# Performance work log

Measured on AMD Instinct MI355X. Metric: run time of the kernel, lower is better.

Reference implementation:

```python
import jax, jax.numpy as jnp
import numpy as np

N_NODES = 50000
N_EDGES = 800000
IN_DIM, HIDDEN, OUT_DIM = 256, 128, 64
N_LAYERS = 2
NEG_SLOPE = 0.1


def setup_inputs() -> dict:
    key = jax.random.key(0)
    ks = jax.random.split(key, 10)
    x = jax.random.normal(ks[0], (N_NODES, IN_DIM), dtype=jnp.float32)
    edge_index = jax.random.randint(ks[1], (2, N_EDGES), 0, N_NODES, dtype=jnp.int64)
    s = 1.0 / np.sqrt(IN_DIM)
    enc_W = jax.random.uniform(ks[2], (IN_DIM, HIDDEN), jnp.float32, -s, s)
    enc_b = jax.random.uniform(ks[3], (HIDDEN,), jnp.float32, -s, s)
    sh = 1.0 / np.sqrt(HIDDEN)
    conv_W = jax.random.uniform(ks[4], (N_LAYERS, HIDDEN, HIDDEN), jnp.float32, -sh, sh)
    conv_b = jnp.zeros((N_LAYERS, HIDDEN), dtype=jnp.float32)
    dec_W = jax.random.uniform(ks[5], (HIDDEN, OUT_DIM), jnp.float32, -sh, sh)
    dec_b = jax.random.uniform(ks[6], (OUT_DIM,), jnp.float32, -sh, sh)
    return {"x": x, "edge_index": edge_index, "enc_W": enc_W, "enc_b": enc_b,
            "conv_W": conv_W, "conv_b": conv_b, "dec_W": dec_W, "dec_b": dec_b}


def _gcn_norm(edge_index, num_nodes):
    # PyG gcn_norm with add_self_loops=True, edge_weight=1
    loops = jnp.arange(num_nodes, dtype=edge_index.dtype)
    src = jnp.concatenate([edge_index[0], loops])
    dst = jnp.concatenate([edge_index[1], loops])
    deg = jax.ops.segment_sum(jnp.ones_like(dst, dtype=jnp.float32), dst,
                              num_segments=num_nodes)
    dinv = jnp.where(deg > 0, jax.lax.rsqrt(deg), 0.0)
    norm = dinv[src] * dinv[dst]  # [E+N]
    return src, dst, norm


def _gcn_conv(h, W, b, src, dst, norm, num_nodes):
    h = h @ W                       # [N, H] dense transform (no bias in lin)
    msg = h[src] * norm[:, None]    # gather + scale, [E+N, H]
    out = jax.ops.segment_sum(msg, dst, num_segments=num_nodes)  # scatter-add
    return out + b


def reference(x, edge_index, enc_W, enc_b, conv_W, conv_b, dec_W, dec_b):
    n = x.shape[0]
    src, dst, norm = _gcn_norm(edge_index, n)
    # eval mode: F.dropout(training=False) is identity
    h = jax.nn.leaky_relu(x @ enc_W + enc_b, NEG_SLOPE)
    for i in range(N_LAYERS):
        h = jax.nn.leaky_relu(_gcn_conv(h, conv_W[i], conv_b[i], src, dst, norm, n),
                              NEG_SLOPE)
    return h @ dec_W + dec_b
```

## Files before the change

kernel.cpp:

```cpp
#include <hip/hip_runtime.h>


constexpr int HID = 128;
constexpr float NEG = 0.1f;
constexpr int CAP = 96;
constexpr int FILL_BLKS = 256;
constexpr int CSTR = 8;

typedef __attribute__((ext_vector_type(8))) short short8;
typedef __attribute__((ext_vector_type(4))) float f32x4;

union frag8 { short8 s; unsigned u[4]; };

__device__ __forceinline__ float lrelu(float v) { return v > 0.f ? v : v * NEG; }

__device__ __forceinline__ unsigned fbits(float f) {
  union { float f; unsigned u; } c; c.f = f; return c.u;
}
__device__ __forceinline__ unsigned short f2bf(float f) {
  unsigned u = fbits(f);
  return (unsigned short)((u + 0x7fffu + ((u >> 16) & 1u)) >> 16);
}
__device__ __forceinline__ float bf2f(unsigned short h) {
  union { unsigned u; float f; } c; c.u = ((unsigned)h) << 16; return c.f;
}

__device__ __forceinline__ void gload16(const unsigned short* g, unsigned short* l) {
  __builtin_amdgcn_global_load_lds((const __attribute__((address_space(1))) unsigned*)g,
                                   (__attribute__((address_space(3))) unsigned*)l, 16, 0, 0);
}

__global__ __launch_bounds__(256) void k_pre(const float* __restrict__ encW,
                                             const float* __restrict__ convW,
                                             const float* __restrict__ decW,
                                             unsigned short* __restrict__ wf_enc,
                                             unsigned short* __restrict__ wf_c0,
                                             unsigned short* __restrict__ wf_c1,
                                             unsigned short* __restrict__ wf_dec,
                                             int* __restrict__ cursor, int N) {
  if (blockIdx.x < 36) {
    int idx = blockIdx.x * 256 + threadIdx.x;
    const float* W; unsigned short* wf; int WN, NT, base, PL;
    if (idx < 4096)      { W = encW;          wf = wf_enc; WN = 128; NT = 8; base = idx;        PL = 32768; }
    else if (idx < 6144) { W = convW;         wf = wf_c0;  WN = 128; NT = 8; base = idx - 4096; PL = 16384; }
    else if (idx < 8192) { W = convW + 16384; wf = wf_c1;  WN = 128; NT = 8; base = idx - 6144; PL = 16384; }
    else if (idx < 9216) { W = decW;          wf = wf_dec; WN = 64;  NT = 4; base = idx - 8192; PL = 8192; }
    else return;
    int lane = base & 63, tile = base >> 6;
    int nt = tile % NT, ks = tile / NT;
    int col = nt * 16 + (lane & 15);
    int krow = ks * 32 + (lane >> 4) * 8;
    unsigned short* ohi = wf + (size_t)base * 8;
    unsigned short* olo = ohi + PL;
#pragma unroll
    for (int j = 0; j < 8; ++j) {
      float v = W[(size_t)(krow + j) * WN + col];
      unsigned short hi = f2bf(v);
      ohi[j] = hi;
      olo[j] = f2bf(v - bf2f(hi));
    }
    return;
  }
  int i = (blockIdx.x - 36) * 256 + threadIdx.x;
  if (i < N) cursor[i * CSTR] = 0;
}

__global__ __launch_bounds__(512) void k_enc_fill(
    const float* __restrict__ A, const unsigned short* __restrict__ wf,
    const float* __restrict__ bias, const int* __restrict__ src,
    const int* __restrict__ dst, int E, int* __restrict__ cursor,
    unsigned short* __restrict__ eidx2, float* __restrict__ h, int M, int encB) {
  __shared__ unsigned short lwf[32768];
  if (blockIdx.x >= encB) {
    int g = blockIdx.x & 7;
    int rk = (blockIdx.x - encB) >> 3;
    int lo = (int)(((long long)g * M) >> 3);
    int hi = (int)(((long long)(g + 1) * M) >> 3);
    for (int e = rk * 512 + threadIdx.x; e < E; e += 32 * 512) {
      int d = dst[e];
      if (d >= lo && d < hi) {
        int pos = atomicAdd(&cursor[d * CSTR], 1);
        if (pos < CAP) eidx2[(size_t)d * CAP + pos] = (unsigned short)src[e];
      }
    }
    return;
  }
  constexpr int NT = 8;
  const int wave = threadIdx.x >> 6, lane = threadIdx.x & 63;
  const int q = lane >> 4, c16 = lane & 15;
  const int row0 = blockIdx.x * 128 + wave * 16;
  int r = row0 + c16;
  if (r >= M) r = M - 1;
  const float* ap = A + (size_t)r * 256 + q * 8;
  f32x4 acc[NT];
#pragma unroll
  for (int nt = 0; nt < NT; ++nt) acc[nt] = (f32x4){0.f, 0.f, 0.f, 0.f};
  float av[8];
  *(float4*)&av[0] = *(const float4*)(ap);
  *(float4*)&av[4] = *(const float4*)(ap + 4);
  for (int half = 0; half < 2; ++half) {
    if (half) __syncthreads();
#pragma unroll
    for (int i = 0; i < 8; ++i) {
      int c = wave + i * 8;
      const unsigned short* s = (c < 32)
          ? wf + half * 16384 + c * 512
          : wf + 32768 + half * 16384 + (c - 32) * 512;
      gload16(s + lane * 8, lwf + c * 512);
    }
    asm volatile("s_waitcnt vmcnt(0)" ::: "memory");
    __syncthreads();
    for (int ksl = 0; ksl < 4; ++ksl) {
      frag8 ahi, alo;
      float res[8];
#pragma unroll
      for (int i = 0; i < 8; ++i) {
        union { unsigned u; float f; } t; t.u = fbits(av[i]) & 0xffff0000u;
        res[i] = av[i] - t.f;
      }
#pragma unroll
      for (int j = 0; j < 4; ++j) {
        ahi.u[j] = __builtin_amdgcn_perm(fbits(av[2 * j + 1]), fbits(av[2 * j]),
                                         0x07060302u);
        alo.u[j] = __builtin_amdgcn_perm(fbits(res[2 * j + 1]), fbits(res[2 * j]),
                                         0x07060302u);
      }
      int ks = half * 4 + ksl;
      if (ks + 1 < 8) {
        *(float4*)&av[0] = *(const float4*)(ap + (ks + 1) * 32);
        *(float4*)&av[4] = *(const float4*)(ap + (ks + 1) * 32 + 4);
      }
      const unsigned short* wph = lwf + ksl * NT * 512 + lane * 8;
#pragma unroll
      for (int nt = 0; nt < NT; ++nt) {
        short8 bhi = *(const short8*)(wph);
        short8 blo = *(const short8*)(wph + 16384);
        acc[nt] = __builtin_amdgcn_mfma_f32_16x16x32_bf16(ahi.s, bhi, acc[nt], 0, 0, 0);
        acc[nt] = __builtin_amdgcn_mfma_f32_16x16x32_bf16(ahi.s, blo, acc[nt], 0, 0, 0);
        acc[nt] = __builtin_amdgcn_mfma_f32_16x16x32_bf16(alo.s, bhi, acc[nt], 0, 0, 0);
        wph += 512;
      }
    }
  }
  float bv[NT];
#pragma unroll
  for (int nt = 0; nt < NT; ++nt) bv[nt] = bias[nt * 16 + c16];
#pragma unroll
  for (int rr = 0; rr < 4; ++rr) {
    int gr = row0 + q * 4 + rr;
    if (gr >= M) continue;
#pragma unroll
    for (int nt = 0; nt < NT; ++nt)
      h[(size_t)gr * 128 + nt * 16 + c16] = lrelu(acc[nt][rr] + bv[nt]);
  }
}

template <int NT, int KS, int MODE>
__global__ __launch_bounds__(512) void k_mfma(const float* __restrict__ A,
                                              const unsigned short* __restrict__ wf,
                                              const float* __restrict__ bias,
                                              const int* __restrict__ deg,
                                              void* __restrict__ Cout, int M) {
  constexpr int K = KS * 32;
  constexpr int NOUT = NT * 16;
  constexpr int PL = KS * NT * 512;
  constexpr int CH = KS * NT * 2;
  __shared__ unsigned short lwf[2 * PL];
  const int wave = threadIdx.x >> 6, lane = threadIdx.x & 63;
  const int q = lane >> 4, c16 = lane & 15;
  const int row0 = blockIdx.x * 128 + wave * 16;
  int r = row0 + c16;
  if (r >= M) r = M - 1;
  const float* ap = A + (size_t)r * K + q * 8;
  f32x4 acc[NT];
#pragma unroll
  for (int nt = 0; nt < NT; ++nt) acc[nt] = (f32x4){0.f, 0.f, 0.f, 0.f};
  float av[8];
  *(float4*)&av[0] = *(const float4*)(ap);
  *(float4*)&av[4] = *(const float4*)(ap + 4);
#pragma unroll
  for (int i = 0; i < CH / 8; ++i) {
    int c = wave + i * 8;
    gload16(wf + c * 512 + lane * 8, lwf + c * 512);
  }
  asm volatile("s_waitcnt vmcnt(0)" ::: "memory");
  __syncthreads();
  for (int ks = 0; ks < KS; ++ks) {
    frag8 ahi, alo;
    float res[8];
#pragma unroll
    for (int i = 0; i < 8; ++i) {
      union { unsigned u; float f; } t; t.u = fbits(av[i]) & 0xffff0000u;
      res[i] = av[i] - t.f;
    }
#pragma unroll
    for (int j = 0; j < 4; ++j) {
      ahi.u[j] = __builtin_amdgcn_perm(fbits(av[2 * j + 1]), fbits(av[2 * j]),
                                       0x07060302u);
      alo.u[j] = __builtin_amdgcn_perm(fbits(res[2 * j + 1]), fbits(res[2 * j]),
                                       0x07060302u);
    }
    if (ks + 1 < KS) {
      *(float4*)&av[0] = *(const float4*)(ap + (ks + 1) * 32);
      *(float4*)&av[4] = *(const float4*)(ap + (ks + 1) * 32 + 4);
    }
    const unsigned short* wph = lwf + ks * NT * 512 + lane * 8;
#pragma unroll
    for (int nt = 0; nt < NT; ++nt) {
      short8 bhi = *(const short8*)(wph);
      short8 blo = *(const short8*)(wph + PL);
      acc[nt] = __builtin_amdgcn_mfma_f32_16x16x32_bf16(ahi.s, bhi, acc[nt], 0, 0, 0);
      acc[nt] = __builtin_amdgcn_mfma_f32_16x16x32_bf16(ahi.s, blo, acc[nt], 0, 0, 0);
      acc[nt] = __builtin_amdgcn_mfma_f32_16x16x32_bf16(alo.s, bhi, acc[nt], 0, 0, 0);
      wph += 512;
    }
  }
  float bv[NT];
  if (MODE == 2) {
#pragma unroll
    for (int nt = 0; nt < NT; ++nt) bv[nt] = bias[nt * 16 + c16];
  }
#pragma unroll
  for (int rr = 0; rr < 4; ++rr) {
    int gr = row0 + q * 4 + rr;
    if (gr >= M) continue;
    if (MODE == 1) {
      float dv = rsqrtf((float)deg[gr * CSTR] + 1.0f);
#pragma unroll
      for (int nt = 0; nt < NT; ++nt)
        ((unsigned short*)Cout)[(size_t)gr * NOUT + nt * 16 + c16] =
            f2bf(acc[nt][rr] * dv);
    } else {
#pragma unroll
      for (int nt = 0; nt < NT; ++nt)
        ((float*)Cout)[(size_t)gr * NOUT + nt * 16 + c16] = acc[nt][rr] + bv[nt];
    }
  }
}

__global__ __launch_bounds__(256) void k_gather(const int* __restrict__ deg,
                                                const unsigned short* __restrict__ eidx2,
                                                const unsigned short* __restrict__ t,
                                                const float* __restrict__ bias,
                                                float* __restrict__ h, int N) {
  int node = (blockIdx.x * 256 + threadIdx.x) >> 4;
  int lane = threadIdx.x & 15;
  if (node >= N) return;
  const uint4* t4 = (const uint4*)t;
  int dtrue = deg[node * CSTR];
  int d = dtrue > CAP ? CAP : dtrue;
  const unsigned short* ep = eidx2 + (size_t)node * CAP;
  float acc[8] = {};
#define ADDV(v)                                         \
  {                                                     \
    unsigned dw[4] = {(v).x, (v).y, (v).z, (v).w};      \
    _Pragma("unroll") for (int i = 0; i < 4; ++i) {     \
      union { unsigned u; float f; } lo, hi;            \
      lo.u = dw[i] << 16;                               \
      hi.u = dw[i] & 0xffff0000u;                       \
      acc[2 * i] += lo.f;                               \
      acc[2 * i + 1] += hi.f;                           \
    }                                                   \
  }
  {
    uint4 vs = t4[(size_t)node * 16 + lane];
    ADDV(vs);
  }
  int e = 0;
  for (; e + 8 <= d; e += 8) {
    int4 sa = *(const int4*)(ep + e);
    unsigned s0 = (unsigned)sa.x & 0xffffu, s1 = (unsigned)sa.x >> 16;
    unsigned s2 = (unsigned)sa.y & 0xffffu, s3 = (unsigned)sa.y >> 16;
    unsigned s4 = (unsigned)sa.z & 0xffffu, s5 = (unsigned)sa.z >> 16;
    unsigned s6 = (unsigned)sa.w & 0xffffu, s7 = (unsigned)sa.w >> 16;
    uint4 v0 = t4[(size_t)s0 * 16 + lane];
    uint4 v1 = t4[(size_t)s1 * 16 + lane];
    uint4 v2 = t4[(size_t)s2 * 16 + lane];
    uint4 v3 = t4[(size_t)s3 * 16 + lane];
    uint4 v4 = t4[(size_t)s4 * 16 + lane];
    uint4 v5 = t4[(size_t)s5 * 16 + lane];
    uint4 v6 = t4[(size_t)s6 * 16 + lane];
    uint4 v7 = t4[(size_t)s7 * 16 + lane];
    ADDV(v0); ADDV(v1); ADDV(v2); ADDV(v3);
    ADDV(v4); ADDV(v5); ADDV(v6); ADDV(v7);
  }
  for (; e < d; ++e) {
    unsigned s = ep[e];
    uint4 v = t4[(size_t)s * 16 + lane];
    ADDV(v);
  }
#undef ADDV
  float w = rsqrtf((float)dtrue + 1.0f);
  float* hp = h + (size_t)node * HID + lane * 8;
  const float* bp = bias + lane * 8;
  float4 o1, o2;
  float* o = (float*)&o1;
#pragma unroll
  for (int i = 0; i < 4; ++i) o[i] = lrelu(acc[i] * w + bp[i]);
  o = (float*)&o2;
#pragma unroll
  for (int i = 0; i < 4; ++i) o[i] = lrelu(acc[4 + i] * w + bp[4 + i]);
  *(float4*)hp = o1;
  *(float4*)(hp + 4) = o2;
}

extern "C" void kernel_launch(void* const* d_in, const int* in_sizes, int n_in,
                              void* d_out, int out_size, void* d_ws, size_t ws_size,
                              hipStream_t stream) {
  const float* x = (const float*)d_in[0];
  const int* ei = (const int*)d_in[1];
  const float* enc_W = (const float*)d_in[2];
  const float* enc_b = (const float*)d_in[3];
  const float* conv_W = (const float*)d_in[4];
  const float* conv_b = (const float*)d_in[5];
  const float* dec_W = (const float*)d_in[6];
  const float* dec_b = (const float*)d_in[7];
  float* out = (float*)d_out;

  const int IN_DIM = 256;
  const int N = in_sizes[0] / IN_DIM;
  const int E = in_sizes[1] / 2;
  const int* src = ei;
  const int* dst = ei + E;

  char* wp = (char*)d_ws;
  auto alloc = [&](size_t bytes) {
    void* p = wp;
    wp += (bytes + 255) & ~(size_t)255;
    return p;
  };
  int* cursor = (int*)alloc((size_t)N * CSTR * 4);
  unsigned short* eidx2 = (unsigned short*)alloc((size_t)N * CAP * 2);
  float* h = (float*)alloc((size_t)N * HID * 4);
  unsigned short* t = (unsigned short*)alloc((size_t)N * HID * 2);
  unsigned short* wf_enc = (unsigned short*)alloc((size_t)8 * 8 * 64 * 16 * 2);
  unsigned short* wf_c0 = (unsigned short*)alloc((size_t)4 * 8 * 64 * 16 * 2);
  unsigned short* wf_c1 = (unsigned short*)alloc((size_t)4 * 8 * 64 * 16 * 2);
  unsigned short* wf_dec = (unsigned short*)alloc((size_t)4 * 4 * 64 * 16 * 2);

  k_pre<<<36 + (N + 255) / 256, 256, 0, stream>>>(enc_W, conv_W, dec_W, wf_enc, wf_c0,
                                                  wf_c1, wf_dec, cursor, N);

  const int encB = (N + 127) / 128;
  k_enc_fill<<<encB + FILL_BLKS, 512, 0, stream>>>(x, wf_enc, enc_b, src, dst, E,
                                                   cursor, eidx2, h, N, encB);

  const int gm = (N + 127) / 128;
  for (int l = 0; l < 2; ++l) {
    const unsigned short* wf = l ? wf_c1 : wf_c0;
    k_mfma<8, 4, 1><<<gm, 512, 0, stream>>>(h, wf, nullptr, cursor, t, N);
    k_gather<<<(N * 16 + 255) / 256, 256, 0, stream>>>(
        cursor, eidx2, t, conv_b + (size_t)l * HID, h, N);
  }

  k_mfma<4, 4, 2><<<gm, 512, 0, stream>>>(h, wf_dec, dec_b, nullptr, out, N);
}
```

Before: 264.7 us.

## Split fused encoder/fill kernel, double-buffer A loads, pad cursor stride

Moves the edge-bucketing atomic fill out of the fused encoder kernel into its own one-thread-per-edge kernel, dropping the 8-way destination-range partitioning. The cursor stride grows from 8 to 32 ints so each node's counter sits on its own cache line, which should reduce atomic contention. The encoder and MFMA kernels now prefetch activation rows two k-steps ahead with a two-slot register buffer and fully unroll the k loop, to hide global load latency. The cost is an extra launch, a larger cursor array, more register pressure, and losing the overlap between the fill and the encoder GEMM.

```diff
diff --git a/kernel.cpp b/kernel.cpp
--- a/kernel.cpp
+++ b/kernel.cpp
@@ -4,8 +4,7 @@
 constexpr int HID = 128;
 constexpr float NEG = 0.1f;
 constexpr int CAP = 96;
-constexpr int FILL_BLKS = 256;
-constexpr int CSTR = 8;
+constexpr int CSTR = 32;
 
 typedef __attribute__((ext_vector_type(8))) short short8;
 typedef __attribute__((ext_vector_type(4))) float f32x4;
@@ -65,26 +64,22 @@
   if (i < N) cursor[i * CSTR] = 0;
 }
 
-__global__ __launch_bounds__(512) void k_enc_fill(
-    const float* __restrict__ A, const unsigned short* __restrict__ wf,
-    const float* __restrict__ bias, const int* __restrict__ src,
-    const int* __restrict__ dst, int E, int* __restrict__ cursor,
-    unsigned short* __restrict__ eidx2, float* __restrict__ h, int M, int encB) {
+__global__ __launch_bounds__(256) void k_fill(const int* __restrict__ src,
+                                              const int* __restrict__ dst, int E,
+                                              int* __restrict__ cursor,
+                                              unsigned short* __restrict__ eidx2) {
+  int e = blockIdx.x * 256 + threadIdx.x;
+  if (e >= E) return;
+  int d = dst[e];
+  int pos = atomicAdd(&cursor[d * CSTR], 1);
+  if (pos < CAP) eidx2[(size_t)d * CAP + pos] = (unsigned short)src[e];
+}
+
+__global__ __launch_bounds__(512) void k_enc(const float* __restrict__ A,
+                                             const unsigned short* __restrict__ wf,
+                                             const float* __restrict__ bias,
+                                             float* __restrict__ h, int M) {
   __shared__ unsigned short lwf[32768];
-  if (blockIdx.x >= encB) {
-    int g = blockIdx.x & 7;
-    int rk = (blockIdx.x - encB) >> 3;
-    int lo = (int)(((long long)g * M) >> 3);
-    int hi = (int)(((long long)(g + 1) * M) >> 3);
-    for (int e = rk * 512 + threadIdx.x; e < E; e += 32 * 512) {
-      int d = dst[e];
-      if (d >= lo && d < hi) {
-        int pos = atomicAdd(&cursor[d * CSTR], 1);
-        if (pos < CAP) eidx2[(size_t)d * CAP + pos] = (unsigned short)src[e];
-      }
-    }
-    return;
-  }
   constexpr int NT = 8;
   const int wave = threadIdx.x >> 6, lane = threadIdx.x & 63;
   const int q = lane >> 4, c16 = lane & 15;
@@ -95,9 +90,11 @@
   f32x4 acc[NT];
 #pragma unroll
   for (int nt = 0; nt < NT; ++nt) acc[nt] = (f32x4){0.f, 0.f, 0.f, 0.f};
-  float av[8];
-  *(float4*)&av[0] = *(const float4*)(ap);
-  *(float4*)&av[4] = *(const float4*)(ap + 4);
+  float av[2][8];
+  *(float4*)&av[0][0] = *(const float4*)(ap);
+  *(float4*)&av[0][4] = *(const float4*)(ap + 4);
+  *(float4*)&av[1][0] = *(const float4*)(ap + 32);
+  *(float4*)&av[1][4] = *(const float4*)(ap + 36);
   for (int half = 0; half < 2; ++half) {
     if (half) __syncthreads();
 #pragma unroll
@@ -110,25 +107,26 @@
     }
     asm volatile("s_waitcnt vmcnt(0)" ::: "memory");
     __syncthreads();
+#pragma unroll
     for (int ksl = 0; ksl < 4; ++ksl) {
       frag8 ahi, alo;
       float res[8];
 #pragma unroll
       for (int i = 0; i < 8; ++i) {
-        union { unsigned u; float f; } t; t.u = fbits(av[i]) & 0xffff0000u;
-        res[i] = av[i] - t.f;
+        union { unsigned u; float f; } t; t.u = fbits(av[ksl & 1][i]) & 0xffff0000u;
+        res[i] = av[ksl & 1][i] - t.f;
       }
 #pragma unroll
       for (int j = 0; j < 4; ++j) {
-        ahi.u[j] = __builtin_amdgcn_perm(fbits(av[2 * j + 1]), fbits(av[2 * j]),
-                                         0x07060302u);
+        ahi.u[j] = __builtin_amdgcn_perm(fbits(av[ksl & 1][2 * j + 1]),
+                                         fbits(av[ksl & 1][2 * j]), 0x07060302u);
         alo.u[j] = __builtin_amdgcn_perm(fbits(res[2 * j + 1]), fbits(res[2 * j]),
                                          0x07060302u);
       }
       int ks = half * 4 + ksl;
-      if (ks + 1 < 8) {
-        *(float4*)&av[0] = *(const float4*)(ap + (ks + 1) * 32);
-        *(float4*)&av[4] = *(const float4*)(ap + (ks + 1) * 32 + 4);
+      if (ks + 2 < 8) {
+        *(float4*)&av[ksl & 1][0] = *(const float4*)(ap + (ks + 2) * 32);
+        *(float4*)&av[ksl & 1][4] = *(const float4*)(ap + (ks + 2) * 32 + 4);
       }
       const unsigned short* wph = lwf + ksl * NT * 512 + lane * 8;
 #pragma unroll
@@ -175,9 +173,13 @@
   f32x4 acc[NT];
 #pragma unroll
   for (int nt = 0; nt < NT; ++nt) acc[nt] = (f32x4){0.f, 0.f, 0.f, 0.f};
-  float av[8];
-  *(float4*)&av[0] = *(const float4*)(ap);
-  *(float4*)&av[4] = *(const float4*)(ap + 4);
+  float av[2][8];
+  *(float4*)&av[0][0] = *(const float4*)(ap);
+  *(float4*)&av[0][4] = *(const float4*)(ap + 4);
+  if (KS > 1) {
+    *(float4*)&av[1][0] = *(const float4*)(ap + 32);
+    *(float4*)&av[1][4] = *(const float4*)(ap + 36);
+  }
 #pragma unroll
   for (int i = 0; i < CH / 8; ++i) {
     int c = wave + i * 8;
@@ -185,24 +187,25 @@
   }
   asm volatile("s_waitcnt vmcnt(0)" ::: "memory");
   __syncthreads();
+#pragma unroll
   for (int ks = 0; ks < KS; ++ks) {
     frag8 ahi, alo;
     float res[8];
 #pragma unroll
     for (int i = 0; i < 8; ++i) {
-      union { unsigned u; float f; } t; t.u = fbits(av[i]) & 0xffff0000u;
-      res[i] = av[i] - t.f;
+      union { unsigned u; float f; } t; t.u = fbits(av[ks & 1][i]) & 0xffff0000u;
+      res[i] = av[ks & 1][i] - t.f;
     }
 #pragma unroll
     for (int j = 0; j < 4; ++j) {
-      ahi.u[j] = __builtin_amdgcn_perm(fbits(av[2 * j + 1]), fbits(av[2 * j]),
-                                       0x07060302u);
+      ahi.u[j] = __builtin_amdgcn_perm(fbits(av[ks & 1][2 * j + 1]),
+                                       fbits(av[ks & 1][2 * j]), 0x07060302u);
       alo.u[j] = __builtin_amdgcn_perm(fbits(res[2 * j + 1]), fbits(res[2 * j]),
                                        0x07060302u);
     }
-    if (ks + 1 < KS) {
-      *(float4*)&av[0] = *(const float4*)(ap + (ks + 1) * 32);
-      *(float4*)&av[4] = *(const float4*)(ap + (ks + 1) * 32 + 4);
+    if (ks + 2 < KS) {
+      *(float4*)&av[ks & 1][0] = *(const float4*)(ap + (ks + 2) * 32);
+      *(float4*)&av[ks & 1][4] = *(const float4*)(ap + (ks + 2) * 32 + 4);
     }
     const unsigned short* wph = lwf + ks * NT * 512 + lane * 8;
 #pragma unroll
@@ -341,9 +344,10 @@
   k_pre<<<36 + (N + 255) / 256, 256, 0, stream>>>(enc_W, conv_W, dec_W, wf_enc, wf_c0,
                                                   wf_c1, wf_dec, cursor, N);
 
+  k_fill<<<(E + 255) / 256, 256, 0, stream>>>(src, dst, E, cursor, eidx2);
+
   const int encB = (N + 127) / 128;
-  k_enc_fill<<<encB + FILL_BLKS, 512, 0, stream>>>(x, wf_enc, enc_b, src, dst, E,
-                                                   cursor, eidx2, h, N, encB);
+  k_enc<<<encB, 512, 0, stream>>>(x, wf_enc, enc_b, h, N);
 
   const int gm = (N + 127) / 128;
   for (int l = 0; l < 2; ++l) {
```

New measurement: 266.3 us. Within noise of the previous version (+0.6%).
